# Performance work log

Hardware: AMD Instinct MI355X
Metric: run time of the kernel (lower is better)

## Reference

```python
import jax, jax.numpy as jnp
import numpy as np

MARGIN = 0.05

def setup_inputs() -> dict:
    key = jax.random.key(0)
    k1, k2 = jax.random.split(key)
    N, D = 8192, 1024
    x = jax.random.normal(k1, (N, D), dtype=jnp.float32)
    y = jax.random.normal(k2, (N, D), dtype=jnp.float32)
    # cosine-style embeddings: L2 normalize
    x = x / jnp.linalg.norm(x, axis=1, keepdims=True)
    y = y / jnp.linalg.norm(y, axis=1, keepdims=True)
    return {"x": x, "y": y}

def reference(x, y):
    N = x.shape[0]
    # positive similarity per pair: [N]
    pos_sim = jnp.sum(x * y, axis=1)
    # hard-negative mining (no gradient through mining)
    xs = jax.lax.stop_gradient(x)
    ys = jax.lax.stop_gradient(y)
    sim = xs @ ys.T  # [N, N]
    diag = jnp.eye(N, dtype=bool)
    diff_neg = (jax.lax.stop_gradient(pos_sim)[:, None] - sim) < 0.0
    masked = jnp.where(diag | diff_neg, jnp.float32(-1.0), sim)
    neg_idx = jnp.argmax(masked, axis=1)  # [N] int
    # negative similarity (gradients flow through x and gathered y rows)
    neg_sim = jnp.sum(x * y[neg_idx], axis=1)
    loss = jnp.mean(jax.nn.relu(MARGIN - pos_sim + neg_sim))
    return loss
```

## Files before the change

### kernel.cpp

```cpp
#include <hip/hip_runtime.h>

#define NROWS 8192
#define DDIM  1024
#define BM 128
#define BN 256
#define BKB 128
#define NSTRIPES 8
#define CT_PER_STRIPE 4
#define MARGIN_F 0.05f
#define FP8_SCALE 8.0f

typedef __attribute__((ext_vector_type(8)))  int   int8v;
typedef __attribute__((ext_vector_type(4)))  int   int4v;
typedef __attribute__((ext_vector_type(16))) float floatx16;

__device__ __forceinline__ void g2lds16(const void* g, void* l) {
  __builtin_amdgcn_global_load_lds(
      (const __attribute__((address_space(1))) void*)g,
      (__attribute__((address_space(3))) void*)l, 16, 0, 0);
}

__device__ __forceinline__ unsigned long long pack_key(float v, int j) {
  unsigned int u = __float_as_uint(v);
  u = (u & 0x80000000u) ? ~u : (u | 0x80000000u);
  return ((unsigned long long)u << 32) | (unsigned long long)(0x7FFFFFFFu - (unsigned int)j);
}

__global__ void prep_kernel(const float* __restrict__ x, const float* __restrict__ y,
                            unsigned int* __restrict__ xq, unsigned int* __restrict__ yq,
                            float* __restrict__ pos, unsigned long long* __restrict__ keys,
                            float* __restrict__ out) {
  const int row = blockIdx.x;
  const int t = threadIdx.x;
  const float4 a = ((const float4*)(x + (size_t)row * DDIM))[t];
  const float4 b = ((const float4*)(y + (size_t)row * DDIM))[t];
  float s = a.x * b.x + a.y * b.y + a.z * b.z + a.w * b.w;

  int pa = __builtin_amdgcn_cvt_pk_fp8_f32(a.x * FP8_SCALE, a.y * FP8_SCALE, 0, false);
  pa     = __builtin_amdgcn_cvt_pk_fp8_f32(a.z * FP8_SCALE, a.w * FP8_SCALE, pa, true);
  int pb = __builtin_amdgcn_cvt_pk_fp8_f32(b.x * FP8_SCALE, b.y * FP8_SCALE, 0, false);
  pb     = __builtin_amdgcn_cvt_pk_fp8_f32(b.z * FP8_SCALE, b.w * FP8_SCALE, pb, true);
  xq[(size_t)row * 256 + t] = (unsigned int)pa;
  yq[(size_t)row * 256 + t] = (unsigned int)pb;

  for (int m = 32; m; m >>= 1) s += __shfl_down(s, m, 64);
  __shared__ float ps[4];
  if ((t & 63) == 0) ps[t >> 6] = s;
  __syncthreads();
  if (t == 0) {
    pos[row] = ps[0] + ps[1] + ps[2] + ps[3];
    keys[row] = 0ULL;
    if (row == 0) out[0] = 0.f;
  }
}

__global__ __launch_bounds__(256, 2) void mine_kernel(
    const unsigned char* __restrict__ xq, const unsigned char* __restrict__ yq,
    const float* __restrict__ pos, unsigned long long* __restrict__ keys) {
  __shared__ unsigned char As[BM * BKB];
  __shared__ unsigned char Bs[BN * BKB];
  __shared__ float pos_s[BM];

  const int t = threadIdx.x;
  const int rowBase = blockIdx.x * BM;
  const int stripe  = blockIdx.y;
  if (t < BM) pos_s[t] = pos[rowBase + t] * (FP8_SCALE * FP8_SCALE);

  const int lane = t & 63;
  const int wave = t >> 6;
  const int wr = wave >> 1, wc = wave & 1;
  const int r31  = lane & 31;
  const int kh   = lane >> 5;
  const int fragOff = ((2 * kh) ^ (r31 & 7)) << 4;
  const int offA0 = (64 * wr + r31) * BKB + fragOff;
  const int offB0 = (128 * wc + r31) * BKB + fragOff;

  for (int ct = 0; ct < CT_PER_STRIPE; ++ct) {
    const int colBase = stripe * (BN * CT_PER_STRIPE) + ct * BN;

    floatx16 acc[2][4];
#pragma unroll
    for (int mi = 0; mi < 2; ++mi)
#pragma unroll
      for (int ni = 0; ni < 4; ++ni)
#pragma unroll
        for (int r = 0; r < 16; ++r) acc[mi][ni][r] = 0.f;

    for (int k0 = 0; k0 < DDIM; k0 += BKB) {
      __syncthreads();
#pragma unroll
      for (int i = 0; i < 4; ++i) {
        const int c  = i * 256 + t;
        const int r  = c >> 3;
        const int sw = (c & 7) ^ (r & 7);
        g2lds16(xq + (size_t)(rowBase + r) * DDIM + k0 + sw * 16,
                &As[(size_t)(i * 256 + wave * 64) * 16]);
      }
#pragma unroll
      for (int i = 0; i < 8; ++i) {
        const int c  = i * 256 + t;
        const int r  = c >> 3;
        const int sw = (c & 7) ^ (r & 7);
        g2lds16(yq + (size_t)(colBase + r) * DDIM + k0 + sw * 16,
                &Bs[(size_t)(i * 256 + wave * 64) * 16]);
      }
      __syncthreads();

#pragma unroll
      for (int ks = 0; ks < 2; ++ks) {
        const int kx = ks << 6;
        int8v af[2];
#pragma unroll
        for (int mi = 0; mi < 2; ++mi) {
          const int oA = (offA0 + mi * 32 * BKB) ^ kx;
          int4v lo = *(const int4v*)&As[oA];
          int4v hi = *(const int4v*)&As[oA ^ 16];
          af[mi] = __builtin_shufflevector(lo, hi, 0, 1, 2, 3, 4, 5, 6, 7);
        }
#pragma unroll
        for (int ni = 0; ni < 4; ++ni) {
          const int oB = (offB0 + ni * 32 * BKB) ^ kx;
          int4v blo = *(const int4v*)&Bs[oB];
          int4v bhi = *(const int4v*)&Bs[oB ^ 16];
          int8v bf = __builtin_shufflevector(blo, bhi, 0, 1, 2, 3, 4, 5, 6, 7);
          acc[0][ni] = __builtin_amdgcn_mfma_scale_f32_32x32x64_f8f6f4(
              af[0], bf, acc[0][ni], 0, 0, 0, 0x7F7F7F7F, 0, 0x7F7F7F7F);
          acc[1][ni] = __builtin_amdgcn_mfma_scale_f32_32x32x64_f8f6f4(
              af[1], bf, acc[1][ni], 0, 0, 0, 0x7F7F7F7F, 0, 0x7F7F7F7F);
        }
      }
    }

#pragma unroll
    for (int mi = 0; mi < 2; ++mi) {
#pragma unroll
      for (int reg = 0; reg < 16; ++reg) {
        const int row_l = 64 * wr + 32 * mi + (reg & 3) + 8 * (reg >> 2) + 4 * kh;
        const int row_g = rowBase + row_l;
        const float p = pos_s[row_l];
        float bestv = -1.0e30f; int bestj = 0;
#pragma unroll
        for (int ni = 0; ni < 4; ++ni) {
          float v = acc[mi][ni][reg];
          const int col_g = colBase + 128 * wc + 32 * ni + r31;
          if (col_g == row_g || v > p) v = -1024.0f;
          if (v > bestv || (v == bestv && col_g < bestj)) { bestv = v; bestj = col_g; }
        }
        unsigned long long key = pack_key(bestv, bestj);
#pragma unroll
        for (int m = 1; m <= 16; m <<= 1) {
          unsigned long long o = __shfl_xor(key, m, 64);
          if (o > key) key = o;
        }
        if (r31 == 0) atomicMax(&keys[row_g], key);
      }
    }
  }
}

__global__ void final_kernel(const float* __restrict__ x, const float* __restrict__ y,
                             const float* __restrict__ pos,
                             const unsigned long long* __restrict__ keys,
                             float* __restrict__ out) {
  const int t = threadIdx.x;
  const int lane = t & 63, wave = t >> 6;
  float accl = 0.f;
#pragma unroll
  for (int i = 0; i < 8; ++i) {
    const int row = blockIdx.x * 32 + i * 4 + wave;
    const unsigned long long k = keys[row];
    const int j = 0x7FFFFFFF - (int)(k & 0xFFFFFFFFULL);
    const float4* xr = (const float4*)(x + (size_t)row * DDIM);
    const float4* yr = (const float4*)(y + (size_t)j * DDIM);
    float s = 0.f;
#pragma unroll
    for (int u = 0; u < 4; ++u) {
      const float4 a = xr[lane + 64 * u];
      const float4 b = yr[lane + 64 * u];
      s += a.x * b.x + a.y * b.y + a.z * b.z + a.w * b.w;
    }
    for (int m = 32; m; m >>= 1) s += __shfl_down(s, m, 64);
    if (lane == 0) {
      const float l = MARGIN_F - pos[row] + s;
      accl += l > 0.f ? l : 0.f;
    }
  }
  __shared__ float ps[4];
  if (lane == 0) ps[wave] = accl;
  __syncthreads();
  if (t == 0) atomicAdd(out, (ps[0] + ps[1] + ps[2] + ps[3]) * (1.0f / (float)NROWS));
}

extern "C" void kernel_launch(void* const* d_in, const int* in_sizes, int n_in,
                              void* d_out, int out_size, void* d_ws, size_t ws_size,
                              hipStream_t stream) {
  const float* x = (const float*)d_in[0];
  const float* y = (const float*)d_in[1];
  float* out = (float*)d_out;

  unsigned long long* keys = (unsigned long long*)d_ws;
  float* pos = (float*)((char*)d_ws + (size_t)NROWS * 8);
  unsigned char* xq = (unsigned char*)d_ws + (size_t)NROWS * 8 + (size_t)NROWS * 4;
  unsigned char* yq = xq + (size_t)NROWS * DDIM;

  prep_kernel<<<NROWS, 256, 0, stream>>>(x, y, (unsigned int*)xq, (unsigned int*)yq,
                                         pos, keys, out);
  dim3 grid(NROWS / BM, NSTRIPES);
  mine_kernel<<<grid, 256, 0, stream>>>(xq, yq, pos, keys);
  final_kernel<<<NROWS / 32, 256, 0, stream>>>(x, y, pos, keys, out);
}
```

Measured before the change: 221.7 us.

## Pack argmax keys to 32 bits, accumulate across tiles, reduce once per row

Mining keys shrink from 64-bit to 32-bit by keeping only the top 19 bits of the order-preserving similarity and putting a 13-bit column index in the low bits. Each thread now keeps a running max key in registers across all column tiles. The cross-lane shuffle reduction and the atomicMax therefore run once per row instead of once per tile. The LDS staging layout is rewritten so fragment reads use plain offsets instead of the XOR swizzle, and the prep kernel now handles one row per wave with no block-level reduction. Truncating the value bits can change tie-breaking between nearly equal similarities.

```diff
diff --git a/kernel.cpp b/kernel.cpp
--- a/kernel.cpp
+++ b/kernel.cpp
@@ -20,43 +20,38 @@
       (__attribute__((address_space(3))) void*)l, 16, 0, 0);
 }
 
-__device__ __forceinline__ unsigned long long pack_key(float v, int j) {
-  unsigned int u = __float_as_uint(v);
-  u = (u & 0x80000000u) ? ~u : (u | 0x80000000u);
-  return ((unsigned long long)u << 32) | (unsigned long long)(0x7FFFFFFFu - (unsigned int)j);
-}
-
 __global__ void prep_kernel(const float* __restrict__ x, const float* __restrict__ y,
                             unsigned int* __restrict__ xq, unsigned int* __restrict__ yq,
-                            float* __restrict__ pos, unsigned long long* __restrict__ keys,
+                            float* __restrict__ pos, unsigned int* __restrict__ keys,
                             float* __restrict__ out) {
-  const int row = blockIdx.x;
   const int t = threadIdx.x;
-  const float4 a = ((const float4*)(x + (size_t)row * DDIM))[t];
-  const float4 b = ((const float4*)(y + (size_t)row * DDIM))[t];
-  float s = a.x * b.x + a.y * b.y + a.z * b.z + a.w * b.w;
-
-  int pa = __builtin_amdgcn_cvt_pk_fp8_f32(a.x * FP8_SCALE, a.y * FP8_SCALE, 0, false);
-  pa     = __builtin_amdgcn_cvt_pk_fp8_f32(a.z * FP8_SCALE, a.w * FP8_SCALE, pa, true);
-  int pb = __builtin_amdgcn_cvt_pk_fp8_f32(b.x * FP8_SCALE, b.y * FP8_SCALE, 0, false);
-  pb     = __builtin_amdgcn_cvt_pk_fp8_f32(b.z * FP8_SCALE, b.w * FP8_SCALE, pb, true);
-  xq[(size_t)row * 256 + t] = (unsigned int)pa;
-  yq[(size_t)row * 256 + t] = (unsigned int)pb;
-
+  const int lane = t & 63, wave = t >> 6;
+  const int row = blockIdx.x * 4 + wave;
+  const float4* xr = (const float4*)(x + (size_t)row * DDIM);
+  const float4* yr = (const float4*)(y + (size_t)row * DDIM);
+  unsigned int* xqr = xq + (size_t)row * 256;
+  unsigned int* yqr = yq + (size_t)row * 256;
+  float s = 0.f;
+#pragma unroll
+  for (int u = 0; u < 4; ++u) {
+    const float4 a = xr[u * 64 + lane];
+    const float4 b = yr[u * 64 + lane];
+    s += a.x * b.x + a.y * b.y + a.z * b.z + a.w * b.w;
+    int pa = __builtin_amdgcn_cvt_pk_fp8_f32(a.x * FP8_SCALE, a.y * FP8_SCALE, 0, false);
+    pa     = __builtin_amdgcn_cvt_pk_fp8_f32(a.z * FP8_SCALE, a.w * FP8_SCALE, pa, true);
+    int pb = __builtin_amdgcn_cvt_pk_fp8_f32(b.x * FP8_SCALE, b.y * FP8_SCALE, 0, false);
+    pb     = __builtin_amdgcn_cvt_pk_fp8_f32(b.z * FP8_SCALE, b.w * FP8_SCALE, pb, true);
+    xqr[u * 64 + lane] = (unsigned int)pa;
+    yqr[u * 64 + lane] = (unsigned int)pb;
+  }
   for (int m = 32; m; m >>= 1) s += __shfl_down(s, m, 64);
-  __shared__ float ps[4];
-  if ((t & 63) == 0) ps[t >> 6] = s;
-  __syncthreads();
-  if (t == 0) {
-    pos[row] = ps[0] + ps[1] + ps[2] + ps[3];
-    keys[row] = 0ULL;
-    if (row == 0) out[0] = 0.f;
-  }
+  if (lane == 0) { pos[row] = s; keys[row] = 0u; }
+  if (blockIdx.x == 0 && t == 0) out[0] = 0.f;
 }
 
 __global__ __launch_bounds__(256, 2) void mine_kernel(
     const unsigned char* __restrict__ xq, const unsigned char* __restrict__ yq,
-    const float* __restrict__ pos, unsigned long long* __restrict__ keys) {
+    const float* __restrict__ pos, unsigned int* __restrict__ keys) {
   __shared__ unsigned char As[BM * BKB];
   __shared__ unsigned char Bs[BN * BKB];
   __shared__ float pos_s[BM];
@@ -69,14 +64,22 @@
   const int lane = t & 63;
   const int wave = t >> 6;
   const int wr = wave >> 1, wc = wave & 1;
-  const int r31  = lane & 31;
-  const int kh   = lane >> 5;
-  const int fragOff = ((2 * kh) ^ (r31 & 7)) << 4;
-  const int offA0 = (64 * wr + r31) * BKB + fragOff;
-  const int offB0 = (128 * wc + r31) * BKB + fragOff;
+  const int r31 = lane & 31, kh = lane >> 5;
+
+  const int rdA = wr * 8192  + lane * 16;
+  const int rdB = wc * 16384 + lane * 16;
+  const int goff = r31 * 1024 + kh * 32 + 16 * (wave & 1);
+  const unsigned char* gA = xq + (size_t)(rowBase + 32 * (wave >> 1)) * 1024 + goff;
+
+  unsigned int key[2][16];
+#pragma unroll
+  for (int mi = 0; mi < 2; ++mi)
+#pragma unroll
+    for (int reg = 0; reg < 16; ++reg) key[mi][reg] = 0u;
 
   for (int ct = 0; ct < CT_PER_STRIPE; ++ct) {
     const int colBase = stripe * (BN * CT_PER_STRIPE) + ct * BN;
+    const unsigned char* gB = yq + (size_t)(colBase + 32 * (wave >> 1)) * 1024 + goff;
 
     floatx16 acc[2][4];
 #pragma unroll
@@ -89,39 +92,28 @@
     for (int k0 = 0; k0 < DDIM; k0 += BKB) {
       __syncthreads();
 #pragma unroll
-      for (int i = 0; i < 4; ++i) {
-        const int c  = i * 256 + t;
-        const int r  = c >> 3;
-        const int sw = (c & 7) ^ (r & 7);
-        g2lds16(xq + (size_t)(rowBase + r) * DDIM + k0 + sw * 16,
-                &As[(size_t)(i * 256 + wave * 64) * 16]);
-      }
-#pragma unroll
-      for (int i = 0; i < 8; ++i) {
-        const int c  = i * 256 + t;
-        const int r  = c >> 3;
-        const int sw = (c & 7) ^ (r & 7);
-        g2lds16(yq + (size_t)(colBase + r) * DDIM + k0 + sw * 16,
-                &Bs[(size_t)(i * 256 + wave * 64) * 16]);
-      }
+      for (int i = 0; i < 4; ++i)
+        g2lds16(gA + (size_t)(64 * (i >> 1)) * 1024 + k0 + 64 * (i & 1),
+                &As[(i * 256 + wave * 64) * 16]);
+#pragma unroll
+      for (int i = 0; i < 8; ++i)
+        g2lds16(gB + (size_t)(128 * (i >> 2) + 64 * (i & 1)) * 1024 + k0 + 64 * ((i >> 1) & 1),
+                &Bs[(i * 256 + wave * 64) * 16]);
       __syncthreads();
 
 #pragma unroll
       for (int ks = 0; ks < 2; ++ks) {
-        const int kx = ks << 6;
         int8v af[2];
 #pragma unroll
         for (int mi = 0; mi < 2; ++mi) {
-          const int oA = (offA0 + mi * 32 * BKB) ^ kx;
-          int4v lo = *(const int4v*)&As[oA];
-          int4v hi = *(const int4v*)&As[oA ^ 16];
+          int4v lo = *(const int4v*)&As[rdA + ks * 4096 + mi * 2048];
+          int4v hi = *(const int4v*)&As[rdA + ks * 4096 + mi * 2048 + 1024];
           af[mi] = __builtin_shufflevector(lo, hi, 0, 1, 2, 3, 4, 5, 6, 7);
         }
 #pragma unroll
         for (int ni = 0; ni < 4; ++ni) {
-          const int oB = (offB0 + ni * 32 * BKB) ^ kx;
-          int4v blo = *(const int4v*)&Bs[oB];
-          int4v bhi = *(const int4v*)&Bs[oB ^ 16];
+          int4v blo = *(const int4v*)&Bs[rdB + ks * 8192 + ni * 2048];
+          int4v bhi = *(const int4v*)&Bs[rdB + ks * 8192 + ni * 2048 + 1024];
           int8v bf = __builtin_shufflevector(blo, bhi, 0, 1, 2, 3, 4, 5, 6, 7);
           acc[0][ni] = __builtin_amdgcn_mfma_scale_f32_32x32x64_f8f6f4(
               af[0], bf, acc[0][ni], 0, 0, 0, 0x7F7F7F7F, 0, 0x7F7F7F7F);
@@ -131,6 +123,9 @@
       }
     }
 
+    int colv[4];
+#pragma unroll
+    for (int ni = 0; ni < 4; ++ni) colv[ni] = colBase + 128 * wc + 32 * ni + r31;
 #pragma unroll
     for (int mi = 0; mi < 2; ++mi) {
 #pragma unroll
@@ -138,21 +133,35 @@
         const int row_l = 64 * wr + 32 * mi + (reg & 3) + 8 * (reg >> 2) + 4 * kh;
         const int row_g = rowBase + row_l;
         const float p = pos_s[row_l];
-        float bestv = -1.0e30f; int bestj = 0;
+        unsigned int kk = key[mi][reg];
 #pragma unroll
         for (int ni = 0; ni < 4; ++ni) {
-          float v = acc[mi][ni][reg];
-          const int col_g = colBase + 128 * wc + 32 * ni + r31;
-          if (col_g == row_g || v > p) v = -1024.0f;
-          if (v > bestv || (v == bestv && col_g < bestj)) { bestv = v; bestj = col_g; }
+          const float v = acc[mi][ni][reg];
+          const bool dead = (colv[ni] == row_g) || (v > p);
+          unsigned int u = __float_as_uint(v);
+          u ^= (unsigned int)(((int)u) >> 31) | 0x80000000u;
+          unsigned int kc = (u & 0xFFFFE000u) | (unsigned int)(8191 - colv[ni]);
+          kc = dead ? 0u : kc;
+          kk = kk > kc ? kk : kc;
         }
-        unsigned long long key = pack_key(bestv, bestj);
-#pragma unroll
-        for (int m = 1; m <= 16; m <<= 1) {
-          unsigned long long o = __shfl_xor(key, m, 64);
-          if (o > key) key = o;
-        }
-        if (r31 == 0) atomicMax(&keys[row_g], key);
+        key[mi][reg] = kk;
+      }
+    }
+  }
+
+#pragma unroll
+  for (int mi = 0; mi < 2; ++mi) {
+#pragma unroll
+    for (int reg = 0; reg < 16; ++reg) {
+      unsigned int kk = key[mi][reg];
+#pragma unroll
+      for (int m = 1; m <= 16; m <<= 1) {
+        unsigned int o = __shfl_xor(kk, m, 64);
+        kk = kk > o ? kk : o;
+      }
+      if (r31 == 0) {
+        const int row_l = 64 * wr + 32 * mi + (reg & 3) + 8 * (reg >> 2) + 4 * kh;
+        atomicMax(&keys[rowBase + row_l], kk);
       }
     }
   }
@@ -160,7 +169,7 @@
 
 __global__ void final_kernel(const float* __restrict__ x, const float* __restrict__ y,
                              const float* __restrict__ pos,
-                             const unsigned long long* __restrict__ keys,
+                             const unsigned int* __restrict__ keys,
                              float* __restrict__ out) {
   const int t = threadIdx.x;
   const int lane = t & 63, wave = t >> 6;
@@ -168,8 +177,8 @@
 #pragma unroll
   for (int i = 0; i < 8; ++i) {
     const int row = blockIdx.x * 32 + i * 4 + wave;
-    const unsigned long long k = keys[row];
-    const int j = 0x7FFFFFFF - (int)(k & 0xFFFFFFFFULL);
+    const unsigned int k = keys[row];
+    const int j = (k == 0u) ? 0 : (8191 - (int)(k & 8191u));
     const float4* xr = (const float4*)(x + (size_t)row * DDIM);
     const float4* yr = (const float4*)(y + (size_t)j * DDIM);
     float s = 0.f;
@@ -198,13 +207,13 @@
   const float* y = (const float*)d_in[1];
   float* out = (float*)d_out;
 
-  unsigned long long* keys = (unsigned long long*)d_ws;
-  float* pos = (float*)((char*)d_ws + (size_t)NROWS * 8);
-  unsigned char* xq = (unsigned char*)d_ws + (size_t)NROWS * 8 + (size_t)NROWS * 4;
+  unsigned int* keys = (unsigned int*)d_ws;
+  float* pos = (float*)((char*)d_ws + (size_t)NROWS * 4);
+  unsigned char* xq = (unsigned char*)d_ws + (size_t)NROWS * 8;
   unsigned char* yq = xq + (size_t)NROWS * DDIM;
 
-  prep_kernel<<<NROWS, 256, 0, stream>>>(x, y, (unsigned int*)xq, (unsigned int*)yq,
-                                         pos, keys, out);
+  prep_kernel<<<NROWS / 4, 256, 0, stream>>>(x, y, (unsigned int*)xq, (unsigned int*)yq,
+                                             pos, keys, out);
   dim3 grid(NROWS / BM, NSTRIPES);
   mine_kernel<<<grid, 256, 0, stream>>>(xq, yq, pos, keys);
   final_kernel<<<NROWS / 32, 256, 0, stream>>>(x, y, pos, keys, out);
```

Result: slower. 258.6 us (+16.7%).
